# Kernel optimization log

Measured on AMD Instinct MI355X. Metric: run time of the kernel, lower is better.

The kernel has to match this reference:

```python
import jax, jax.numpy as jnp
import numpy as np

N, LAT, H, R, L = 384, 64, 128, 16, 3
CUTOFF = 12.0
COORD_INIT_SCALE = 0.001


def setup_inputs() -> dict:
    key = jax.random.key(0)
    ks = jax.random.split(key, 12)
    def w(k, shape, fan):
        return jax.random.normal(k, shape, jnp.float32) / np.float32(np.sqrt(fan))
    return {
        "z": jax.random.normal(ks[0], (N, LAT), jnp.float32),
        # spread anchors so the radius graph is non-trivially sparse
        "anchor_coords": jax.random.normal(ks[1], (N, 3), jnp.float32) * 10.0,
        "proj_W": w(ks[2], (LAT, H), LAT),
        "proj_b": jnp.zeros((H,), jnp.float32),
        "eW1": w(ks[3], (L, 2 * H + R, H), 2 * H + R),
        "eb1": jnp.zeros((L, H), jnp.float32),
        "eW2": w(ks[4], (L, H, H), H),
        "eb2": jnp.zeros((L, H), jnp.float32),
        "nW1": w(ks[5], (L, 2 * H, H), 2 * H),
        "nb1": jnp.zeros((L, H), jnp.float32),
        "nW2": w(ks[6], (L, H, H), H),
        "nb2": jnp.zeros((L, H), jnp.float32),
        "cW1": w(ks[7], (L, H, H), H),
        "cb1": jnp.zeros((L, H), jnp.float32),
        # coord head scaled by coord_update_init_scale for stable coordinate updates
        "cW2": w(ks[8], (L, H, 1), H) * COORD_INIT_SCALE,
    }


def _rbf(d):
    # Gaussian radial basis expansion over [0, cutoff]
    mu = jnp.linspace(0.0, CUTOFF, R, dtype=d.dtype)            # (R,)
    gamma = jnp.asarray((R / CUTOFF) ** 2, d.dtype)
    return jnp.exp(-gamma * (d[..., None] - mu) ** 2)           # (..., R)


def reference(z, anchor_coords, proj_W, proj_b, eW1, eb1, eW2, eb2,
              nW1, nb1, nW2, nb2, cW1, cb1, cW2):
    silu = jax.nn.silu
    n = z.shape[0]
    h = z @ proj_W + proj_b                                      # (N, H)
    x = anchor_coords - anchor_coords.mean(0, keepdims=True)     # (N, 3)

    idx = jnp.arange(n)
    seq_mask = jnp.abs(idx[:, None] - idx[None, :]) == 1         # sequential edges
    eye = jnp.eye(n, dtype=bool)

    for l in range(L):
        # rebuild radius graph from current coords (dense jit-safe mask)
        diff = x[:, None, :] - x[None, :, :]                     # (N, N, 3) x_i - x_j
        d2 = jnp.sum(diff * diff, axis=-1)                       # (N, N)
        mask = ((d2 < CUTOFF ** 2) & ~eye) | seq_mask            # (N, N) bool
        maskf = mask.astype(h.dtype)
        d = jnp.sqrt(jnp.where(mask, d2, 1.0)) * maskf           # NaN-safe sqrt
        e = _rbf(d)                                              # (N, N, R)

        hi = jnp.broadcast_to(h[:, None, :], (n, n, H))          # receiver
        hj = jnp.broadcast_to(h[None, :, :], (n, n, H))          # sender
        m = silu(jnp.concatenate([hi, hj, e], -1) @ eW1[l] + eb1[l])
        m = silu(m @ eW2[l] + eb2[l]) * maskf[..., None]         # (N, N, H) messages

        agg = m.sum(1)                                           # scatter-add at receiver
        h = h + silu(jnp.concatenate([h, agg], -1) @ nW1[l] + nb1[l]) @ nW2[l] + nb2[l]

        w = (silu(m @ cW1[l] + cb1[l]) @ cW2[l]) * maskf[..., None]  # (N, N, 1)
        x = x + jnp.sum(diff * w, axis=1)                        # equivariant coord update
    return x
```

## Files before the change

### kernel.cpp

```cpp
#include <hip/hip_runtime.h>
#include <hip/hip_bf16.h>

#define NN 384
#define CUTOFF2 144.0f
#define GAMMA 1.7777778f

#define PK_L 26624
#define PK_WE 8192
#define PK_W2 10240
#define PK_C1 18432

#define STG_F32 1152
#define SCRATCH_B (8*STG_F32*4)
#define PERSIST_OFF (PK_L*4 + SCRATCH_B)
#define K_SMEM (PERSIST_OFF + 15408)

#define O_H    9216
#define O_A    205824
#define O_XA   0
#define O_XB   4608
#define O_HBF0 599040
#define O_HBF1 697344
#define O_MEAN 3076112
#define O_PK   3076160

typedef __bf16 bf16x8 __attribute__((ext_vector_type(8)));
typedef float f32x4 __attribute__((ext_vector_type(4)));

union ER { struct { float dx, dy, dz; unsigned j; } e; uint4 u4; };

__device__ __forceinline__ unsigned short f2bf(float f){
  unsigned u = __float_as_uint(f);
  return (unsigned short)((u + 0x7fffu + ((u >> 16) & 1u)) >> 16);
}
__device__ __forceinline__ unsigned pk2(float a, float b){
  return ((unsigned)f2bf(b) << 16) | f2bf(a);
}
__device__ __forceinline__ float silu(float x){ return x / (1.0f + __expf(-x)); }

__device__ __forceinline__ void scan_rows(
    int row, int rowsel, int t256, bool v, const float* __restrict__ x,
    uint4* sEr, int* pCnt){
  int* scnt = &pCnt[rowsel];
  if (t256 == 0) *scnt = 0;
  __syncthreads();
  if (v) {
    float xi0 = x[row*3], xi1 = x[row*3+1], xi2 = x[row*3+2];
    for (int j = t256; j < 384; j += 256) {
      float d0 = xi0-x[j*3], d1 = xi1-x[j*3+1], d2 = xi2-x[j*3+2];
      float dd = d0*d0 + d1*d1 + d2*d2;
      bool msk = ((dd < CUTOFF2) && (j != row)) || (j == row-1) || (j == row+1);
      if (msk) {
        int ss = atomicAdd(scnt, 1);
        ER er; er.e.dx = d0; er.e.dy = d1; er.e.dz = d2; er.e.j = (unsigned)j;
        sEr[rowsel*384 + ss] = er.u4;
      }
    }
  }
  __syncthreads();
  if (v) {
    int cnt = *scnt;
    int p = (32 - (cnt & 31)) & 31;
    if (t256 < p) {
      ER er; er.e.dx = 0.f; er.e.dy = 0.f; er.e.dz = 0.f; er.e.j = (unsigned)row;
      sEr[rowsel*384 + cnt + t256] = er.u4;
    }
  }
}

#define TRANSFORM(VA, VB, FA, FB)                                              \
  _Pragma("unroll")                                                            \
  for (int c = 0; c < 4; ++c) {                                                \
    _Pragma("unroll")                                                          \
    for (int tl = 0; tl < 2; ++tl) {                                           \
      int t = 2*c + tl;                                                        \
      _Pragma("unroll")                                                        \
      for (int r = 0; r < 4; ++r) {                                            \
        stg[(quad*4 + r)*36 + tl*16 + col0] = VA[t][r];                        \
        stg[(16 + quad*4 + r)*36 + tl*16 + col0] = VB[t][r];                   \
      }                                                                        \
    }                                                                          \
    float4 lo = *(const float4*)(stg + col0*36 + quad*8);                      \
    float4 hi = *(const float4*)(stg + col0*36 + quad*8 + 4);                  \
    FA[c].u = make_uint4(pk2(lo.x,lo.y), pk2(lo.z,lo.w),                       \
                         pk2(hi.x,hi.y), pk2(hi.z,hi.w));                      \
    float4 lo2 = *(const float4*)(stg + (16 + col0)*36 + quad*8);              \
    float4 hi2 = *(const float4*)(stg + (16 + col0)*36 + quad*8 + 4);          \
    FB[c].u = make_uint4(pk2(lo2.x,lo2.y), pk2(lo2.z,lo2.w),                   \
                         pk2(hi2.x,hi2.y), pk2(hi2.z,hi2.w));                  \
  }

__device__ __forceinline__ void edge_phase(
    const unsigned short* __restrict__ hbf,
    const unsigned* smem, float* scratch,
    const float* pSa, float* pSg, float* pDx, const int* pCnt, const uint4* sEr,
    const float* __restrict__ eb2g, const float* __restrict__ cb1g,
    const float* __restrict__ cw2g, int valid1){
  const int tid = threadIdx.x, q = tid & 63, s = tid >> 6;
  const int col0 = q & 15, quad = q >> 4;
  float eb2v[8], cb1v[8], cw2v[8];
  #pragma unroll
  for (int t = 0; t < 8; ++t) {
    int c = t*16 + col0;
    eb2v[t] = eb2g[c]; cb1v[t] = cb1g[c]; cw2v[t] = cw2g[c];
  }
  float* stg = scratch + s*STG_F32;
  const f32x4 z4 = {0.f, 0.f, 0.f, 0.f};
  union U8 { uint4 u; bf16x8 v; };

  const int nu0 = (pCnt[0] + 31) >> 5;
  const int nu1 = valid1 ? ((pCnt[1] + 31) >> 5) : 0;
  const int nu = nu0 + nu1;

  for (int k = s; k < nu; k += 8) {
    const int rs = (k < nu0) ? 0 : 1;
    const int ub = (k < nu0) ? k : k - nu0;
    int nvalid = pCnt[rs] - ub*32; if (nvalid > 32) nvalid = 32;
    float Aval[8];
    #pragma unroll
    for (int t = 0; t < 8; ++t) Aval[t] = pSa[rs*128 + t*16 + col0];
    ER e0, e1;
    e0.u4 = sEr[rs*384 + ub*32 + col0];
    e1.u4 = sEr[rs*384 + ub*32 + 16 + col0];
    const int j0 = (int)e0.e.j, j1 = (int)e1.e.j;
    const float d0x = e0.e.dx, d0y = e0.e.dy, d0z = e0.e.dz;
    const float d1x = e1.e.dx, d1y = e1.e.dy, d1z = e1.e.dz;
    const float dd0 = sqrtf(d0x*d0x + d0y*d0y + d0z*d0z);
    const float dd1 = sqrtf(d1x*d1x + d1y*d1y + d1z*d1z);

    U8 ha0[4], ha1[4];
    #pragma unroll
    for (int c = 0; c < 4; ++c) {
      ha0[c].u = *(const uint4*)(hbf + j0*128 + c*32 + quad*8);
      ha1[c].u = *(const uint4*)(hbf + j1*128 + c*32 + quad*8);
    }

    U8 cve0, cve1;
    if (q < 32) {
      #pragma unroll
      for (int tp = 0; tp < 4; ++tp) {
        float k0 = (float)(quad*8 + 2*tp);
        float t00 = dd0 - 0.8f*k0, t01 = dd0 - 0.8f*(k0+1.f);
        float t10 = dd1 - 0.8f*k0, t11 = dd1 - 0.8f*(k0+1.f);
        (&cve0.u.x)[tp] = pk2(__expf(-GAMMA*t00*t00), __expf(-GAMMA*t01*t01));
        (&cve1.u.x)[tp] = pk2(__expf(-GAMMA*t10*t10), __expf(-GAMMA*t11*t11));
      }
    } else { cve0.u = make_uint4(0,0,0,0); cve1.u = make_uint4(0,0,0,0); }

    f32x4 acc0[8], acc1[8];
    #pragma unroll
    for (int t = 0; t < 8; ++t) { acc0[t] = z4; acc1[t] = z4; }
    #pragma unroll
    for (int t = 0; t < 8; ++t) {
      #pragma unroll
      for (int c = 0; c < 4; ++c) {
        bf16x8 w = *(const bf16x8*)(smem + ((t*4 + c)*64 + q)*4);
        acc0[t] = __builtin_amdgcn_mfma_f32_16x16x32_bf16(ha0[c].v, w, acc0[t], 0, 0, 0);
        acc1[t] = __builtin_amdgcn_mfma_f32_16x16x32_bf16(ha1[c].v, w, acc1[t], 0, 0, 0);
      }
      bf16x8 we = *(const bf16x8*)(smem + PK_WE + (t*64 + q)*4);
      acc0[t] = __builtin_amdgcn_mfma_f32_16x16x32_bf16(cve0.v, we, acc0[t], 0, 0, 0);
      acc1[t] = __builtin_amdgcn_mfma_f32_16x16x32_bf16(cve1.v, we, acc1[t], 0, 0, 0);
    }
    #pragma unroll
    for (int t = 0; t < 8; ++t)
      #pragma unroll
      for (int r = 0; r < 4; ++r) {
        acc0[t][r] = silu(acc0[t][r] + Aval[t]);
        acc1[t][r] = silu(acc1[t][r] + Aval[t]);
      }

    U8 a20[4], a21[4];
    TRANSFORM(acc0, acc1, a20, a21);

    f32x4 m0[8], m1v[8];
    #pragma unroll
    for (int t = 0; t < 8; ++t) { m0[t] = z4; m1v[t] = z4; }
    #pragma unroll
    for (int t = 0; t < 8; ++t)
      #pragma unroll
      for (int c = 0; c < 4; ++c) {
        bf16x8 w = *(const bf16x8*)(smem + PK_W2 + ((t*4 + c)*64 + q)*4);
        m0[t] = __builtin_amdgcn_mfma_f32_16x16x32_bf16(a20[c].v, w, m0[t], 0, 0, 0);
        m1v[t] = __builtin_amdgcn_mfma_f32_16x16x32_bf16(a21[c].v, w, m1v[t], 0, 0, 0);
      }
    #pragma unroll
    for (int t = 0; t < 8; ++t) {
      float cs = 0.f;
      #pragma unroll
      for (int r = 0; r < 4; ++r) {
        m0[t][r] = silu(m0[t][r] + eb2v[t]);
        m1v[t][r] = silu(m1v[t][r] + eb2v[t]);
        if (quad*4 + r < nvalid) cs += m0[t][r];
        if (16 + quad*4 + r < nvalid) cs += m1v[t][r];
      }
      cs += __shfl_xor(cs, 16); cs += __shfl_xor(cs, 32);
      if (q < 16) atomicAdd(&pSg[rs*128 + t*16 + q], cs);
    }

    U8 a30[4], a31[4];
    TRANSFORM(m0, m1v, a30, a31);

    f32x4 c30[8], c31[8];
    #pragma unroll
    for (int t = 0; t < 8; ++t) { c30[t] = z4; c31[t] = z4; }
    #pragma unroll
    for (int t = 0; t < 8; ++t)
      #pragma unroll
      for (int c = 0; c < 4; ++c) {
        bf16x8 w = *(const bf16x8*)(smem + PK_C1 + ((t*4 + c)*64 + q)*4);
        c30[t] = __builtin_amdgcn_mfma_f32_16x16x32_bf16(a30[c].v, w, c30[t], 0, 0, 0);
        c31[t] = __builtin_amdgcn_mfma_f32_16x16x32_bf16(a31[c].v, w, c31[t], 0, 0, 0);
      }
    float p0[4], p1[4];
    #pragma unroll
    for (int r = 0; r < 4; ++r) {
      float pa = 0.f, pb = 0.f;
      #pragma unroll
      for (int t = 0; t < 8; ++t) {
        pa += silu(c30[t][r] + cb1v[t]) * cw2v[t];
        pb += silu(c31[t][r] + cb1v[t]) * cw2v[t];
      }
      if (quad*4 + r >= nvalid) pa = 0.f;
      if (16 + quad*4 + r >= nvalid) pb = 0.f;
      p0[r] = pa; p1[r] = pb;
    }
    #pragma unroll
    for (int r = 0; r < 4; ++r)
      #pragma unroll
      for (int off = 1; off < 16; off <<= 1) {
        p0[r] += __shfl_xor(p0[r], off);
        p1[r] += __shfl_xor(p1[r], off);
      }
    float dx0 = 0.f, dx1 = 0.f, dx2 = 0.f;
    #pragma unroll
    for (int r = 0; r < 4; ++r) {
      int el = quad*4 + r;
      float s0 = __shfl(d0x, el), s1 = __shfl(d0y, el), s2 = __shfl(d0z, el);
      if (col0 == 0) { dx0 += p0[r]*s0; dx1 += p0[r]*s1; dx2 += p0[r]*s2; }
      float u0 = __shfl(d1x, el), u1 = __shfl(d1y, el), u2 = __shfl(d1z, el);
      if (col0 == 0) { dx0 += p1[r]*u0; dx1 += p1[r]*u1; dx2 += p1[r]*u2; }
    }
    dx0 += __shfl_xor(dx0, 16); dx0 += __shfl_xor(dx0, 32);
    dx1 += __shfl_xor(dx1, 16); dx1 += __shfl_xor(dx1, 32);
    dx2 += __shfl_xor(dx2, 16); dx2 += __shfl_xor(dx2, 32);
    if (q == 0) {
      atomicAdd(&pDx[rs*4 + 0], dx0);
      atomicAdd(&pDx[rs*4 + 1], dx1);
      atomicAdd(&pDx[rs*4 + 2], dx2);
    }
  }
}

__device__ __forceinline__ void node_phase(
    const float* __restrict__ nW1l, const float* __restrict__ nb1l,
    const float* __restrict__ nW2l, const float* __restrict__ nb2l,
    const float* __restrict__ eW1n, const float* __restrict__ eb1n,
    unsigned short* __restrict__ hbf_out,
    float* __restrict__ hg, float* __restrict__ Ag,
    float* pSh, float* pSa, const float* pSg,
    float* scratch, int rowsel, int half, int o, int row, bool v){
  float* sb = scratch + rowsel*768;
  float* st = sb; float* part = sb + 128;

  float aa = 0.f;
  if (v) {
    const float* src = half ? (pSg + rowsel*128) : (pSh + rowsel*128);
    const float* wb  = nW1l + half*128*128;
    float a0=0,a1=0,a2=0,a3=0;
    #pragma unroll 16
    for (int k = 0; k < 128; k += 4) {
      a0 += src[k]   * wb[k*128 + o];
      a1 += src[k+1] * wb[(k+1)*128 + o];
      a2 += src[k+2] * wb[(k+2)*128 + o];
      a3 += src[k+3] * wb[(k+3)*128 + o];
    }
    aa = (a0+a1)+(a2+a3);
    if (half) part[o] = aa;
  }
  __syncthreads();
  if (v && !half) st[o] = silu(nb1l[o] + aa + part[o]);
  __syncthreads();
  float bb = 0.f;
  if (v) {
    int k0 = half*64;
    float b0=0,b1=0,b2=0,b3=0;
    #pragma unroll 16
    for (int k = k0; k < k0+64; k += 4) {
      b0 += st[k]   * nW2l[k*128 + o];
      b1 += st[k+1] * nW2l[(k+1)*128 + o];
      b2 += st[k+2] * nW2l[(k+2)*128 + o];
      b3 += st[k+3] * nW2l[(k+3)*128 + o];
    }
    bb = (b0+b1)+(b2+b3);
    if (half) part[o] = bb;
  }
  __syncthreads();
  if (v && !half) {
    float hn = pSh[rowsel*128 + o] + nb2l[o] + bb + part[o];
    pSh[rowsel*128 + o] = hn;
    hg[row*128 + o] = hn;
    hbf_out[row*128 + o] = f2bf(hn);
  }
  __syncthreads();
  float cc = 0.f;
  if (v) {
    const float* shn = pSh + rowsel*128;
    int k0 = half*64;
    float c0=0,c1=0,c2=0,c3=0;
    #pragma unroll 16
    for (int k = k0; k < k0+64; k += 4) {
      c0 += shn[k]   * eW1n[k*128 + o];
      c1 += shn[k+1] * eW1n[(k+1)*128 + o];
      c2 += shn[k+2] * eW1n[(k+2)*128 + o];
      c3 += shn[k+3] * eW1n[(k+3)*128 + o];
    }
    cc = (c0+c1)+(c2+c3);
    if (half) part[o] = cc;
  }
  __syncthreads();
  if (v && !half) Ag[row*128 + o] = eb1n[o] + cc + part[o];
}

__global__ __launch_bounds__(512) void k_init(
    const float* __restrict__ eW1, const float* __restrict__ eW2,
    const float* __restrict__ cW1, unsigned* __restrict__ pk,
    const float* __restrict__ anchor, const float* __restrict__ z,
    const float* __restrict__ pW, const float* __restrict__ pbias,
    const float* __restrict__ eb1, float* __restrict__ h,
    unsigned short* __restrict__ hbf, float* __restrict__ A,
    float* __restrict__ meanw){
  __shared__ float sb2[2*768];
  __shared__ float ssum[3];
  const int b = blockIdx.x, tid = threadIdx.x;
  const int rowsel = tid >> 8, half = (tid >> 7) & 1, o = tid & 127;
  {
    int t = b*512 + tid;
    if (t < 3*PK_L) {
      int layer = t / PK_L, r = t % PK_L;
      const float* src; int fr; int isWe = 0;
      if (r < PK_WE)        { fr = r;          src = eW1 + (layer*272 + 128)*128; }
      else if (r < PK_W2)   { fr = r - PK_WE;  src = eW1 + (layer*272 + 256)*128; isWe = 1; }
      else if (r < PK_C1)   { fr = r - PK_W2;  src = eW2 + layer*128*128; }
      else                  { fr = r - PK_C1;  src = cW1 + layer*128*128; }
      int tp = fr & 3, ll = (fr >> 2) & 63, nc = fr >> 8;
      int n, k;
      if (!isWe) { n = nc >> 2; int c = nc & 3; k = c*32 + ((ll>>4)<<3) + 2*tp; }
      else       { n = nc;                      k = ((ll>>4)<<3) + 2*tp; }
      int nn2 = n*16 + (ll & 15);
      float w0, w1;
      if (isWe) { w0 = (k < 16)   ? src[k*128+nn2]     : 0.f;
                  w1 = (k+1 < 16) ? src[(k+1)*128+nn2] : 0.f; }
      else      { w0 = src[k*128+nn2]; w1 = src[(k+1)*128+nn2]; }
      pk[t] = ((unsigned)f2bf(w1) << 16) | f2bf(w0);
    }
  }
  if (b == 0) {
    if (tid < 3) ssum[tid] = 0.f;
    __syncthreads();
    if (tid < 384) {
      atomicAdd(&ssum[0], anchor[tid*3]);
      atomicAdd(&ssum[1], anchor[tid*3+1]);
      atomicAdd(&ssum[2], anchor[tid*3+2]);
    }
    __syncthreads();
    if (tid < 3) meanw[tid] = ssum[tid]*(1.f/384.f);
  }
  const int row = b + 256*rowsel;
  const bool v = row < NN;
  float* sb = sb2 + rowsel*768;
  float* sh = sb; float* part = sb + 512; float* sz = sb + 640;
  if (v && half == 0 && o < 64) sz[o] = z[row*64 + o];
  __syncthreads();
  float pp = 0.f;
  if (v) {
    int k0 = half*32;
    float p0=0,p1=0,p2=0,p3=0;
    #pragma unroll 8
    for (int k = k0; k < k0+32; k += 4) {
      p0 += sz[k]   * pW[k*128 + o];
      p1 += sz[k+1] * pW[(k+1)*128 + o];
      p2 += sz[k+2] * pW[(k+2)*128 + o];
      p3 += sz[k+3] * pW[(k+3)*128 + o];
    }
    pp = (p0+p1)+(p2+p3);
    if (half) part[o] = pp;
  }
  __syncthreads();
  if (v && !half) {
    float hh = pbias[o] + pp + part[o];
    h[row*128 + o] = hh; sh[o] = hh;
    hbf[row*128 + o] = f2bf(hh);
  }
  __syncthreads();
  float cc = 0.f;
  if (v) {
    int k0 = half*64;
    float c0=0,c1=0,c2=0,c3=0;
    #pragma unroll 16
    for (int k = k0; k < k0+64; k += 4) {
      c0 += sh[k]   * eW1[k*128 + o];
      c1 += sh[k+1] * eW1[(k+1)*128 + o];
      c2 += sh[k+2] * eW1[(k+2)*128 + o];
      c3 += sh[k+3] * eW1[(k+3)*128 + o];
    }
    cc = (c0+c1)+(c2+c3);
    if (half) part[o] = cc;
  }
  __syncthreads();
  if (v && !half) A[row*128 + o] = eb1[o] + cc + part[o];
}

__global__ __launch_bounds__(512, 1) void k_layer(
    const unsigned* __restrict__ pkl,
    const float* __restrict__ x_src, float* __restrict__ x_dst,
    const unsigned short* __restrict__ hbf_in, unsigned short* __restrict__ hbf_out,
    float* __restrict__ h, float* __restrict__ A,
    const float* __restrict__ eb2l, const float* __restrict__ cb1l,
    const float* __restrict__ cw2l,
    const float* __restrict__ nW1l, const float* __restrict__ nb1l,
    const float* __restrict__ nW2l, const float* __restrict__ nb2l,
    const float* __restrict__ eW1n, const float* __restrict__ eb1n,
    const float* __restrict__ meanp, int do_node){
  extern __shared__ unsigned smem[];
  const int b = blockIdx.x, tid = threadIdx.x;
  const int rowsel = tid >> 8, half = (tid >> 7) & 1, o = tid & 127, t256 = tid & 255;
  const int row = b + 256*rowsel;
  const bool v = row < NN;
  float* scratch = (float*)(smem + PK_L);
  char* pb8 = (char*)smem + PERSIST_OFF;
  float* pSh = (float*)pb8;
  float* pSa = pSh + 256;
  float* pSg = pSa + 256;
  float* pDx = pSg + 256;
  int*   pCnt = (int*)(pDx + 8);
  uint4* sEr = (uint4*)(pb8 + 3120);

  #pragma unroll
  for (int idx = tid; idx < PK_L/4; idx += 512)
    __builtin_amdgcn_global_load_lds(
        (const __attribute__((address_space(1))) unsigned*)(pkl + idx*4),
        (__attribute__((address_space(3))) unsigned*)(smem + idx*4),
        16, 0, 0);
  if (tid < 256) {
    int rr = b + 256*(tid >> 7);
    if (rr < NN) {
      pSh[tid] = h[rr*128 + (tid & 127)];
      pSa[tid] = A[rr*128 + (tid & 127)];
    }
    pSg[tid] = 0.f;
  } else if (tid < 264) pDx[tid - 256] = 0.f;
  scan_rows(row, rowsel, t256, v, x_src, sEr, pCnt);
  __syncthreads();
  edge_phase(hbf_in, smem, scratch, pSa, pSg, pDx, pCnt, sEr,
             eb2l, cb1l, cw2l, b < 128);
  __syncthreads();
  if (v && half == 0 && o < 3) {
    float xn = x_src[row*3 + o] + pDx[rowsel*4 + o];
    x_dst[row*3 + o] = meanp ? (xn - meanp[o]) : xn;
  }
  if (do_node)
    node_phase(nW1l, nb1l, nW2l, nb2l, eW1n, eb1n, hbf_out, h, A,
               pSh, pSa, pSg, scratch, rowsel, half, o, row, v);
}

extern "C" void kernel_launch(void* const* d_in, const int* in_sizes, int n_in,
                              void* d_out, int out_size, void* d_ws, size_t ws_size,
                              hipStream_t stream){
  const float* z      = (const float*)d_in[0];
  const float* anchor = (const float*)d_in[1];
  const float* projW  = (const float*)d_in[2];
  const float* projb  = (const float*)d_in[3];
  const float* eW1    = (const float*)d_in[4];
  const float* eb1    = (const float*)d_in[5];
  const float* eW2    = (const float*)d_in[6];
  const float* eb2    = (const float*)d_in[7];
  const float* nW1    = (const float*)d_in[8];
  const float* nb1    = (const float*)d_in[9];
  const float* nW2    = (const float*)d_in[10];
  const float* nb2    = (const float*)d_in[11];
  const float* cW1    = (const float*)d_in[12];
  const float* cb1    = (const float*)d_in[13];
  const float* cW2    = (const float*)d_in[14];
  float* out = (float*)d_out;

  char* w = (char*)d_ws;
  float* xA  = (float*)(w + O_XA);
  float* xB  = (float*)(w + O_XB);
  float* h   = (float*)(w + O_H);
  float* A   = (float*)(w + O_A);
  unsigned short* hbf0 = (unsigned short*)(w + O_HBF0);
  unsigned short* hbf1 = (unsigned short*)(w + O_HBF1);
  float* meanw = (float*)(w + O_MEAN);
  unsigned* pk = (unsigned*)(w + O_PK);

  hipFuncSetAttribute((const void*)k_layer, hipFuncAttributeMaxDynamicSharedMemorySize, K_SMEM);

  k_init<<<256, 512, 0, stream>>>(eW1, eW2, cW1, pk, anchor, z, projW, projb,
                                  eb1, h, hbf0, A, meanw);
  k_layer<<<256, 512, K_SMEM, stream>>>(pk, anchor, xB, hbf0, hbf1, h, A,
      eb2, cb1, cW2,
      nW1, nb1, nW2, nb2, eW1 + 272*128, eb1 + 128,
      (const float*)nullptr, 1);
  k_layer<<<256, 512, K_SMEM, stream>>>(pk + PK_L, xB, xA, hbf1, hbf0, h, A,
      eb2 + 128, cb1 + 128, cW2 + 128,
      nW1 + 256*128, nb1 + 128, nW2 + 128*128, nb2 + 128,
      eW1 + 2*272*128, eb1 + 256,
      (const float*)nullptr, 1);
  k_layer<<<256, 512, K_SMEM, stream>>>(pk + 2*PK_L, xA, out, hbf0, hbf1, h, A,
      eb2 + 256, cb1 + 256, cW2 + 256,
      nW1, nb1, nW2, nb2, eW1, eb1,
      meanw, 0);
}
```

Before: 172.4 us.

## Double k_layer block to 1024 threads with 16 edge waves and 4-way node split

Result: slower. 210.1 us (+21.9%).

```diff
diff --git a/kernel.cpp b/kernel.cpp
--- a/kernel.cpp
+++ b/kernel.cpp
@@ -10,8 +10,8 @@
 #define PK_W2 10240
 #define PK_C1 18432
 
-#define STG_F32 1152
-#define SCRATCH_B (8*STG_F32*4)
+#define STG_F32 576
+#define SCRATCH_B (16*STG_F32*4)
 #define PERSIST_OFF (PK_L*4 + SCRATCH_B)
 #define K_SMEM (PERSIST_OFF + 15408)
 
@@ -38,56 +38,59 @@
 }
 __device__ __forceinline__ float silu(float x){ return x / (1.0f + __expf(-x)); }
 
-__device__ __forceinline__ void scan_rows(
-    int row, int rowsel, int t256, bool v, const float* __restrict__ x,
+__device__ __forceinline__ void scan_rows2(
+    int row, int rsel, int t512, bool v, const float* __restrict__ x,
     uint4* sEr, int* pCnt){
-  int* scnt = &pCnt[rowsel];
-  if (t256 == 0) *scnt = 0;
+  if (t512 == 0) pCnt[rsel] = 0;
+  __syncthreads();
+  if (v && t512 < 384) {
+    int j = t512;
+    float xi0 = x[row*3], xi1 = x[row*3+1], xi2 = x[row*3+2];
+    float d0 = xi0-x[j*3], d1 = xi1-x[j*3+1], d2 = xi2-x[j*3+2];
+    float dd = d0*d0 + d1*d1 + d2*d2;
+    bool msk = ((dd < CUTOFF2) && (j != row)) || (j == row-1) || (j == row+1);
+    if (msk) {
+      int ss = atomicAdd(&pCnt[rsel], 1);
+      ER er; er.e.dx = d0; er.e.dy = d1; er.e.dz = d2; er.e.j = (unsigned)j;
+      sEr[rsel*384 + ss] = er.u4;
+    }
+  }
   __syncthreads();
   if (v) {
-    float xi0 = x[row*3], xi1 = x[row*3+1], xi2 = x[row*3+2];
-    for (int j = t256; j < 384; j += 256) {
-      float d0 = xi0-x[j*3], d1 = xi1-x[j*3+1], d2 = xi2-x[j*3+2];
-      float dd = d0*d0 + d1*d1 + d2*d2;
-      bool msk = ((dd < CUTOFF2) && (j != row)) || (j == row-1) || (j == row+1);
-      if (msk) {
-        int ss = atomicAdd(scnt, 1);
-        ER er; er.e.dx = d0; er.e.dy = d1; er.e.dz = d2; er.e.j = (unsigned)j;
-        sEr[rowsel*384 + ss] = er.u4;
-      }
-    }
-  }
-  __syncthreads();
-  if (v) {
-    int cnt = *scnt;
+    int cnt = pCnt[rsel];
     int p = (32 - (cnt & 31)) & 31;
-    if (t256 < p) {
+    if (t512 < p) {
       ER er; er.e.dx = 0.f; er.e.dy = 0.f; er.e.dz = 0.f; er.e.j = (unsigned)row;
-      sEr[rowsel*384 + cnt + t256] = er.u4;
-    }
-  }
-}
-
-#define TRANSFORM(VA, VB, FA, FB)                                              \
+      sEr[rsel*384 + cnt + t512] = er.u4;
+    }
+  }
+}
+
+#define TRANSFORM2(VA, VB, FA, FB)                                             \
   _Pragma("unroll")                                                            \
   for (int c = 0; c < 4; ++c) {                                                \
     _Pragma("unroll")                                                          \
     for (int tl = 0; tl < 2; ++tl) {                                           \
       int t = 2*c + tl;                                                        \
       _Pragma("unroll")                                                        \
-      for (int r = 0; r < 4; ++r) {                                            \
+      for (int r = 0; r < 4; ++r)                                              \
         stg[(quad*4 + r)*36 + tl*16 + col0] = VA[t][r];                        \
-        stg[(16 + quad*4 + r)*36 + tl*16 + col0] = VB[t][r];                   \
-      }                                                                        \
     }                                                                          \
-    float4 lo = *(const float4*)(stg + col0*36 + quad*8);                      \
-    float4 hi = *(const float4*)(stg + col0*36 + quad*8 + 4);                  \
-    FA[c].u = make_uint4(pk2(lo.x,lo.y), pk2(lo.z,lo.w),                       \
-                         pk2(hi.x,hi.y), pk2(hi.z,hi.w));                      \
-    float4 lo2 = *(const float4*)(stg + (16 + col0)*36 + quad*8);              \
-    float4 hi2 = *(const float4*)(stg + (16 + col0)*36 + quad*8 + 4);          \
-    FB[c].u = make_uint4(pk2(lo2.x,lo2.y), pk2(lo2.z,lo2.w),                   \
-                         pk2(hi2.x,hi2.y), pk2(hi2.z,hi2.w));                  \
+    { float4 lo = *(const float4*)(stg + col0*36 + quad*8);                    \
+      float4 hi = *(const float4*)(stg + col0*36 + quad*8 + 4);                \
+      FA[c].u = make_uint4(pk2(lo.x,lo.y), pk2(lo.z,lo.w),                     \
+                           pk2(hi.x,hi.y), pk2(hi.z,hi.w)); }                  \
+    _Pragma("unroll")                                                          \
+    for (int tl = 0; tl < 2; ++tl) {                                           \
+      int t = 2*c + tl;                                                        \
+      _Pragma("unroll")                                                        \
+      for (int r = 0; r < 4; ++r)                                              \
+        stg[(quad*4 + r)*36 + tl*16 + col0] = VB[t][r];                        \
+    }                                                                          \
+    { float4 lo2 = *(const float4*)(stg + col0*36 + quad*8);                   \
+      float4 hi2 = *(const float4*)(stg + col0*36 + quad*8 + 4);               \
+      FB[c].u = make_uint4(pk2(lo2.x,lo2.y), pk2(lo2.z,lo2.w),                 \
+                           pk2(hi2.x,hi2.y), pk2(hi2.z,hi2.w)); }              \
   }
 
 __device__ __forceinline__ void edge_phase(
@@ -112,7 +115,7 @@
   const int nu1 = valid1 ? ((pCnt[1] + 31) >> 5) : 0;
   const int nu = nu0 + nu1;
 
-  for (int k = s; k < nu; k += 8) {
+  for (int k = s; k < nu; k += 16) {
     const int rs = (k < nu0) ? 0 : 1;
     const int ub = (k < nu0) ? k : k - nu0;
     int nvalid = pCnt[rs] - ub*32; if (nvalid > 32) nvalid = 32;
@@ -171,7 +174,7 @@
       }
 
     U8 a20[4], a21[4];
-    TRANSFORM(acc0, acc1, a20, a21);
+    TRANSFORM2(acc0, acc1, a20, a21);
 
     f32x4 m0[8], m1v[8];
     #pragma unroll
@@ -199,7 +202,7 @@
     }
 
     U8 a30[4], a31[4];
-    TRANSFORM(m0, m1v, a30, a31);
+    TRANSFORM2(m0, m1v, a30, a31);
 
     f32x4 c30[8], c31[8];
     #pragma unroll
@@ -252,74 +255,77 @@
   }
 }
 
-__device__ __forceinline__ void node_phase(
+__device__ __forceinline__ void node_phase4(
     const float* __restrict__ nW1l, const float* __restrict__ nb1l,
     const float* __restrict__ nW2l, const float* __restrict__ nb2l,
     const float* __restrict__ eW1n, const float* __restrict__ eb1n,
     unsigned short* __restrict__ hbf_out,
     float* __restrict__ hg, float* __restrict__ Ag,
     float* pSh, float* pSa, const float* pSg,
-    float* scratch, int rowsel, int half, int o, int row, bool v){
-  float* sb = scratch + rowsel*768;
-  float* st = sb; float* part = sb + 128;
+    float* nodeScr, int rsel, int q4, int o, int row, bool v){
+  float* st   = nodeScr + rsel*512;
+  float* part = st + 128;
 
   float aa = 0.f;
   if (v) {
-    const float* src = half ? (pSg + rowsel*128) : (pSh + rowsel*128);
-    const float* wb  = nW1l + half*128*128;
+    int kb = q4*64;
+    const float* srcv = (q4 < 2) ? (pSh + rsel*128) : (pSg + rsel*128);
+    int off = (q4 < 2) ? kb : kb - 128;
     float a0=0,a1=0,a2=0,a3=0;
-    #pragma unroll 16
-    for (int k = 0; k < 128; k += 4) {
-      a0 += src[k]   * wb[k*128 + o];
-      a1 += src[k+1] * wb[(k+1)*128 + o];
-      a2 += src[k+2] * wb[(k+2)*128 + o];
-      a3 += src[k+3] * wb[(k+3)*128 + o];
+    #pragma unroll 8
+    for (int i = 0; i < 64; i += 4) {
+      a0 += srcv[off+i]   * nW1l[(kb+i)*128 + o];
+      a1 += srcv[off+i+1] * nW1l[(kb+i+1)*128 + o];
+      a2 += srcv[off+i+2] * nW1l[(kb+i+2)*128 + o];
+      a3 += srcv[off+i+3] * nW1l[(kb+i+3)*128 + o];
     }
     aa = (a0+a1)+(a2+a3);
-    if (half) part[o] = aa;
-  }
-  __syncthreads();
-  if (v && !half) st[o] = silu(nb1l[o] + aa + part[o]);
+    if (q4) part[(q4-1)*128 + o] = aa;
+  }
+  __syncthreads();
+  if (v && q4 == 0)
+    st[o] = silu(nb1l[o] + aa + part[o] + part[128+o] + part[256+o]);
   __syncthreads();
   float bb = 0.f;
   if (v) {
-    int k0 = half*64;
+    int kb = q4*32;
     float b0=0,b1=0,b2=0,b3=0;
-    #pragma unroll 16
-    for (int k = k0; k < k0+64; k += 4) {
-      b0 += st[k]   * nW2l[k*128 + o];
-      b1 += st[k+1] * nW2l[(k+1)*128 + o];
-      b2 += st[k+2] * nW2l[(k+2)*128 + o];
-      b3 += st[k+3] * nW2l[(k+3)*128 + o];
+    #pragma unroll 8
+    for (int i = 0; i < 32; i += 4) {
+      b0 += st[kb+i]   * nW2l[(kb+i)*128 + o];
+      b1 += st[kb+i+1] * nW2l[(kb+i+1)*128 + o];
+      b2 += st[kb+i+2] * nW2l[(kb+i+2)*128 + o];
+      b3 += st[kb+i+3] * nW2l[(kb+i+3)*128 + o];
     }
     bb = (b0+b1)+(b2+b3);
-    if (half) part[o] = bb;
-  }
-  __syncthreads();
-  if (v && !half) {
-    float hn = pSh[rowsel*128 + o] + nb2l[o] + bb + part[o];
-    pSh[rowsel*128 + o] = hn;
+    if (q4) part[(q4-1)*128 + o] = bb;
+  }
+  __syncthreads();
+  if (v && q4 == 0) {
+    float hn = pSh[rsel*128 + o] + nb2l[o] + bb + part[o] + part[128+o] + part[256+o];
+    pSh[rsel*128 + o] = hn;
     hg[row*128 + o] = hn;
     hbf_out[row*128 + o] = f2bf(hn);
   }
   __syncthreads();
   float cc = 0.f;
   if (v) {
-    const float* shn = pSh + rowsel*128;
-    int k0 = half*64;
+    const float* shn = pSh + rsel*128;
+    int kb = q4*32;
     float c0=0,c1=0,c2=0,c3=0;
-    #pragma unroll 16
-    for (int k = k0; k < k0+64; k += 4) {
-      c0 += shn[k]   * eW1n[k*128 + o];
-      c1 += shn[k+1] * eW1n[(k+1)*128 + o];
-      c2 += shn[k+2] * eW1n[(k+2)*128 + o];
-      c3 += shn[k+3] * eW1n[(k+3)*128 + o];
+    #pragma unroll 8
+    for (int i = 0; i < 32; i += 4) {
+      c0 += shn[kb+i]   * eW1n[(kb+i)*128 + o];
+      c1 += shn[kb+i+1] * eW1n[(kb+i+1)*128 + o];
+      c2 += shn[kb+i+2] * eW1n[(kb+i+2)*128 + o];
+      c3 += shn[kb+i+3] * eW1n[(kb+i+3)*128 + o];
     }
     cc = (c0+c1)+(c2+c3);
-    if (half) part[o] = cc;
-  }
-  __syncthreads();
-  if (v && !half) Ag[row*128 + o] = eb1n[o] + cc + part[o];
+    if (q4) part[(q4-1)*128 + o] = cc;
+  }
+  __syncthreads();
+  if (v && q4 == 0)
+    Ag[row*128 + o] = eb1n[o] + cc + part[o] + part[128+o] + part[256+o];
 }
 
 __global__ __launch_bounds__(512) void k_init(
@@ -411,7 +417,7 @@
   if (v && !half) A[row*128 + o] = eb1[o] + cc + part[o];
 }
 
-__global__ __launch_bounds__(512, 1) void k_layer(
+__global__ __launch_bounds__(1024) void k_layer(
     const unsigned* __restrict__ pkl,
     const float* __restrict__ x_src, float* __restrict__ x_dst,
     const unsigned short* __restrict__ hbf_in, unsigned short* __restrict__ hbf_out,
@@ -424,8 +430,9 @@
     const float* __restrict__ meanp, int do_node){
   extern __shared__ unsigned smem[];
   const int b = blockIdx.x, tid = threadIdx.x;
-  const int rowsel = tid >> 8, half = (tid >> 7) & 1, o = tid & 127, t256 = tid & 255;
-  const int row = b + 256*rowsel;
+  const int rsel = tid >> 9, t512 = tid & 511;
+  const int q4 = (tid >> 7) & 3, o = tid & 127;
+  const int row = b + 256*rsel;
   const bool v = row < NN;
   float* scratch = (float*)(smem + PK_L);
   char* pb8 = (char*)smem + PERSIST_OFF;
@@ -436,8 +443,7 @@
   int*   pCnt = (int*)(pDx + 8);
   uint4* sEr = (uint4*)(pb8 + 3120);
 
-  #pragma unroll
-  for (int idx = tid; idx < PK_L/4; idx += 512)
+  for (int idx = tid; idx < PK_L/4; idx += 1024)
     __builtin_amdgcn_global_load_lds(
         (const __attribute__((address_space(1))) unsigned*)(pkl + idx*4),
         (__attribute__((address_space(3))) unsigned*)(smem + idx*4),
@@ -450,18 +456,18 @@
     }
     pSg[tid] = 0.f;
   } else if (tid < 264) pDx[tid - 256] = 0.f;
-  scan_rows(row, rowsel, t256, v, x_src, sEr, pCnt);
+  scan_rows2(row, rsel, t512, v, x_src, sEr, pCnt);
   __syncthreads();
   edge_phase(hbf_in, smem, scratch, pSa, pSg, pDx, pCnt, sEr,
              eb2l, cb1l, cw2l, b < 128);
   __syncthreads();
-  if (v && half == 0 && o < 3) {
-    float xn = x_src[row*3 + o] + pDx[rowsel*4 + o];
-    x_dst[row*3 + o] = meanp ? (xn - meanp[o]) : xn;
+  if (v && t512 < 3) {
+    float xn = x_src[row*3 + t512] + pDx[rsel*4 + t512];
+    x_dst[row*3 + t512] = meanp ? (xn - meanp[t512]) : xn;
   }
   if (do_node)
-    node_phase(nW1l, nb1l, nW2l, nb2l, eW1n, eb1n, hbf_out, h, A,
-               pSh, pSa, pSg, scratch, rowsel, half, o, row, v);
+    node_phase4(nW1l, nb1l, nW2l, nb2l, eW1n, eb1n, hbf_out, h, A,
+                pSh, pSa, pSg, scratch, rsel, q4, o, row, v);
 }
 
 extern "C" void kernel_launch(void* const* d_in, const int* in_sizes, int n_in,
@@ -498,16 +504,16 @@
 
   k_init<<<256, 512, 0, stream>>>(eW1, eW2, cW1, pk, anchor, z, projW, projb,
                                   eb1, h, hbf0, A, meanw);
-  k_layer<<<256, 512, K_SMEM, stream>>>(pk, anchor, xB, hbf0, hbf1, h, A,
+  k_layer<<<256, 1024, K_SMEM, stream>>>(pk, anchor, xB, hbf0, hbf1, h, A,
       eb2, cb1, cW2,
       nW1, nb1, nW2, nb2, eW1 + 272*128, eb1 + 128,
       (const float*)nullptr, 1);
-  k_layer<<<256, 512, K_SMEM, stream>>>(pk + PK_L, xB, xA, hbf1, hbf0, h, A,
+  k_layer<<<256, 1024, K_SMEM, stream>>>(pk + PK_L, xB, xA, hbf1, hbf0, h, A,
       eb2 + 128, cb1 + 128, cW2 + 128,
       nW1 + 256*128, nb1 + 128, nW2 + 128*128, nb2 + 128,
       eW1 + 2*272*128, eb1 + 256,
       (const float*)nullptr, 1);
-  k_layer<<<256, 512, K_SMEM, stream>>>(pk + 2*PK_L, xA, out, hbf0, hbf1, h, A,
+  k_layer<<<256, 1024, K_SMEM, stream>>>(pk + 2*PK_L, xA, out, hbf0, hbf1, h, A,
       eb2 + 256, cb1 + 256, cW2 + 256,
       nW1, nb1, nW2, nb2, eW1, eb1,
       meanw, 0);
```
